# Kernel optimization log

Measured on AMD Instinct MI355X. Metric: run time of the kernel, lower is better.

The kernel has to match this reference:

```python
import jax, jax.numpy as jnp
import numpy as np

B, S, D_MODEL, D_OUT = 4, 4096, 512, 64


def setup_inputs() -> dict:
    key = jax.random.key(0)
    ks = jax.random.split(key, 10)
    query = jax.random.normal(ks[0], (B, S, D_MODEL), dtype=jnp.float32)
    key_t = jax.random.normal(ks[1], (B, S, D_MODEL), dtype=jnp.float32)
    value = jax.random.normal(ks[2], (B, S, D_MODEL), dtype=jnp.float32)
    mask = jax.random.randint(ks[3], (B, S, S), 0, 2, dtype=jnp.int32)
    sc = 1.0 / np.sqrt(D_MODEL)
    Wq = jax.random.uniform(ks[4], (D_MODEL, D_OUT), minval=-sc, maxval=sc, dtype=jnp.float32)
    bq = jnp.zeros((D_OUT,), dtype=jnp.float32)
    Wk = jax.random.uniform(ks[5], (D_MODEL, D_OUT), minval=-sc, maxval=sc, dtype=jnp.float32)
    bk = jnp.zeros((D_OUT,), dtype=jnp.float32)
    Wv = jax.random.uniform(ks[6], (D_MODEL, D_OUT), minval=-sc, maxval=sc, dtype=jnp.float32)
    bv = jnp.zeros((D_OUT,), dtype=jnp.float32)
    return {"query": query, "key": key_t, "value": value, "mask": mask,
            "Wq": Wq, "bq": bq, "Wk": Wk, "bk": bk, "Wv": Wv, "bv": bv}


def reference(query, key, value, mask, Wq, bq, Wk, bk, Wv, bv):
    # Linear projections (single head): [B,S,D_MODEL] @ [D_MODEL,D_OUT] + bias
    q = jnp.einsum('bsd,de->bse', query, Wq) + bq
    k = jnp.einsum('bsd,de->bse', key, Wk) + bk
    v = jnp.einsum('bsd,de->bse', value, Wv) + bv
    dim_k = k.shape[-1]
    scores = jnp.einsum('bqe,bke->bqk', q, k) / jnp.sqrt(jnp.float32(dim_k))  # [B,S,S]
    scores = jnp.where(mask == 0, -jnp.inf, scores)
    weights = jax.nn.softmax(scores, axis=-1)
    # dropout is identity in eval mode / for deterministic reference
    outputs = jnp.einsum('bqk,bke->bqe', weights, v)  # [B,S,D_OUT]
    return outputs
```

## Files before the change

kernel.cpp:

```cpp
#include <hip/hip_runtime.h>
#include <hip/hip_bf16.h>

#define BB 4
#define SS 4096
#define DMODEL 512
#define DOUT 64
#define NKH 2
#define KH (SS / NKH)
#define NIT (KH / 64)

typedef __bf16 bf16_t;
typedef __bf16 bf16x8 __attribute__((ext_vector_type(8)));
typedef float floatx4 __attribute__((ext_vector_type(4)));

__device__ inline void gl_lds16(const void* g, void* l) {
  __builtin_amdgcn_global_load_lds(
      (const __attribute__((address_space(1))) unsigned int*)g,
      (__attribute__((address_space(3))) unsigned int*)l, 16, 0, 0);
}

__global__ __launch_bounds__(256) void wtrans_kernel(
    const float* __restrict__ Wq, const float* __restrict__ Wk,
    const float* __restrict__ Wv, bf16_t* __restrict__ wT) {
  int idx = blockIdx.x * 256 + threadIdx.x;
  int mat = idx >> 12;
  int r   = idx & 4095;
  int e   = r & 63;
  int d0  = (r >> 6) << 3;
  const float* W = (mat == 0) ? Wq : ((mat == 1) ? Wk : Wv);
  bf16_t* dst = wT + (size_t)mat * (DOUT * DMODEL) + (size_t)e * DMODEL + d0;
#pragma unroll
  for (int j = 0; j < 8; ++j) dst[j] = (bf16_t)W[(size_t)(d0 + j) * DOUT + e];
}

__global__ __launch_bounds__(256) void proj_kernel(
    const float* __restrict__ inq, const float* __restrict__ ink,
    const float* __restrict__ inv, const bf16_t* __restrict__ wT,
    const float* __restrict__ bq, const float* __restrict__ bk,
    const float* __restrict__ bv,
    bf16_t* __restrict__ q_ws, bf16_t* __restrict__ k_ws,
    bf16_t* __restrict__ v_wsT) {
  const int mat = blockIdx.x >> 8;
  const int s0  = (blockIdx.x & 255) << 6;
  const int lane = threadIdx.x & 63;
  const int w    = threadIdx.x >> 6;
  const int col  = lane & 15, quad = lane >> 4;

  const float* inp  = (mat == 0) ? inq : ((mat == 1) ? ink : inv);
  const float* bias = (mat == 0) ? bq : ((mat == 1) ? bk : bv);
  const bf16_t* wt  = wT + (size_t)mat * (DOUT * DMODEL);

  const int arow = s0 + w * 16 + col;
  floatx4 acc[4] = {};

  for (int ch = 0; ch < 16; ++ch) {
    const int d0 = ch * 32 + quad * 8;
    float4 a0 = *(const float4*)(inp + (size_t)arow * DMODEL + d0);
    float4 a1 = *(const float4*)(inp + (size_t)arow * DMODEL + d0 + 4);
    bf16x8 af;
    af[0] = (bf16_t)a0.x; af[1] = (bf16_t)a0.y; af[2] = (bf16_t)a0.z; af[3] = (bf16_t)a0.w;
    af[4] = (bf16_t)a1.x; af[5] = (bf16_t)a1.y; af[6] = (bf16_t)a1.z; af[7] = (bf16_t)a1.w;
#pragma unroll
    for (int c = 0; c < 4; ++c) {
      bf16x8 bw = *(const bf16x8*)(wt + (size_t)(c * 16 + col) * DMODEL + d0);
      acc[c] = __builtin_amdgcn_mfma_f32_16x16x32_bf16(af, bw, acc[c], 0, 0, 0);
    }
  }

#pragma unroll
  for (int c = 0; c < 4; ++c) {
    float bcol = bias[c * 16 + col];
#pragma unroll
    for (int r = 0; r < 4; ++r) {
      int row = s0 + w * 16 + quad * 4 + r;
      float v = acc[c][r] + bcol;
      if (mat == 2) {
        int b = row >> 12, sp = row & 4095;
        v_wsT[((size_t)(b * DOUT + c * 16 + col)) * SS + sp] = (bf16_t)v;
      } else {
        bf16_t* dst = (mat == 0) ? q_ws : k_ws;
        dst[(size_t)row * DOUT + c * 16 + col] = (bf16_t)v;
      }
    }
  }
}

__global__ __launch_bounds__(256, 2) void attn_kernel(
    const bf16_t* __restrict__ q_ws, const bf16_t* __restrict__ k_ws,
    const bf16_t* __restrict__ v_wsT, const int* __restrict__ mask,
    float* __restrict__ O_part, float* __restrict__ l_part) {
  const int bq = blockIdx.x >> 1, kh = blockIdx.x & 1;
  const int b  = bq >> 6;
  const int q0 = (bq & 63) << 6;
  const int kbase = kh * KH;
  const int lane = threadIdx.x & 63;
  const int wi   = threadIdx.x >> 6;
  const int col  = lane & 15, quad = lane >> 4;

  __shared__ __align__(16) bf16_t Kb[2][64 * 64];
  __shared__ __align__(16) bf16_t Vb[2][64 * 64];
  __shared__ __align__(16) bf16_t Pl[4][16][72];

  const int qrowA = q0 + wi * 16 + col;
  const bf16_t* qbase = q_ws + ((size_t)(b * SS) + qrowA) * DOUT + quad * 8;
  const bf16x8 qa0 = *(const bf16x8*)(qbase);
  const bf16x8 qa1 = *(const bf16x8*)(qbase + 32);
  const int* mrow = mask + ((size_t)(b * SS) + qrowA) * SS + quad * 8;

  const int srow = lane >> 3;
  const int schk = (lane & 7) ^ srow;

  auto stage = [&](int it, int buf) {
    const int k0 = kbase + it * 64;
#pragma unroll
    for (int j = 0; j < 2; ++j) {
      const int i = wi * 2 + j;
      const int r = i * 8 + srow;
      const char* gK = (const char*)(k_ws + ((size_t)(b * SS) + k0 + r) * DOUT) + schk * 16;
      gl_lds16(gK, (char*)(&Kb[buf][0]) + i * 1024);
      const char* gV = (const char*)(v_wsT + ((size_t)(b * DOUT) + r) * SS + k0) + schk * 16;
      gl_lds16(gV, (char*)(&Vb[buf][0]) + i * 1024);
    }
  };

  int4 mc[2][2], mn[2][2];
  auto loadM = [&](int k0, int4 m[2][2]) {
#pragma unroll
    for (int s = 0; s < 2; ++s) {
      const int4* mp = (const int4*)(mrow + k0 + s * 32);
      m[s][0] = mp[0];
      m[s][1] = mp[1];
    }
  };

  floatx4 o[4] = {};
  float l_acc = 0.f;
  const bf16_t* prow_r = &Pl[wi][col][quad * 8];

  stage(0, 0);
  loadM(kbase, mc);
  __syncthreads();

  for (int it = 0; it < NIT; ++it) {
    const int buf = it & 1;
    const int itn = (it + 1 < NIT) ? it + 1 : it;

    loadM(kbase + itn * 64, mn);
    stage(itn, buf ^ 1);

    floatx4 sacc[4];
#pragma unroll
    for (int c = 0; c < 4; ++c) {
      const int row = c * 16 + col;
      bf16x8 k0f = *(const bf16x8*)((const char*)&Kb[buf][0] + row * 128 + ((quad ^ (col & 7)) * 16));
      bf16x8 k1f = *(const bf16x8*)((const char*)&Kb[buf][0] + row * 128 + (((4 | quad) ^ (col & 7)) * 16));
      floatx4 z = {};
      z = __builtin_amdgcn_mfma_f32_16x16x32_bf16(qa0, k0f, z, 0, 0, 0);
      z = __builtin_amdgcn_mfma_f32_16x16x32_bf16(qa1, k1f, z, 0, 0, 0);
      sacc[c] = z;
    }

    bf16x8 vc[4][2];
#pragma unroll
    for (int c = 0; c < 4; ++c) {
      const int row = c * 16 + col;
      vc[c][0] = *(const bf16x8*)((const char*)&Vb[buf][0] + row * 128 + ((quad ^ (col & 7)) * 16));
      vc[c][1] = *(const bf16x8*)((const char*)&Vb[buf][0] + row * 128 + (((4 | quad) ^ (col & 7)) * 16));
    }

#pragma unroll
    for (int c = 0; c < 4; ++c)
#pragma unroll
      for (int r = 0; r < 4; ++r)
        Pl[wi][quad * 4 + r][c * 16 + col] = (bf16_t)__expf(sacc[c][r] * 0.125f);

    asm volatile("s_waitcnt lgkmcnt(0)" ::: "memory");

    bf16x8 pa0 = *(const bf16x8*)(prow_r);
    bf16x8 pa1 = *(const bf16x8*)(prow_r + 32);

    float lp = 0.f;
    bf16x8 pm0, pm1;
    auto apply = [&](bf16x8 pa, int4 mlo, int4 mhi, bf16x8& pm) {
      int mm[8] = {mlo.x, mlo.y, mlo.z, mlo.w, mhi.x, mhi.y, mhi.z, mhi.w};
#pragma unroll
      for (int j = 0; j < 8; ++j) {
        bf16_t pv = (mm[j] != 0) ? pa[j] : (bf16_t)0.0f;
        pm[j] = pv;
        lp += (float)pv;
      }
    };
    apply(pa0, mc[0][0], mc[0][1], pm0);
    apply(pa1, mc[1][0], mc[1][1], pm1);
    lp += __shfl_xor(lp, 16);
    lp += __shfl_xor(lp, 32);
    l_acc += lp;

#pragma unroll
    for (int c = 0; c < 4; ++c) {
      o[c] = __builtin_amdgcn_mfma_f32_16x16x32_bf16(pm0, vc[c][0], o[c], 0, 0, 0);
      o[c] = __builtin_amdgcn_mfma_f32_16x16x32_bf16(pm1, vc[c][1], o[c], 0, 0, 0);
    }

    mc[0][0] = mn[0][0]; mc[0][1] = mn[0][1];
    mc[1][0] = mn[1][0]; mc[1][1] = mn[1][1];

    __syncthreads();
  }

  float* Op = O_part + (size_t)blockIdx.x * 64 * 64;
#pragma unroll
  for (int c = 0; c < 4; ++c)
#pragma unroll
    for (int r = 0; r < 4; ++r)
      Op[(wi * 16 + quad * 4 + r) * 64 + c * 16 + col] = o[c][r];
  if (quad == 0) l_part[(size_t)blockIdx.x * 64 + wi * 16 + col] = l_acc;
}

__global__ __launch_bounds__(256) void combine_kernel(
    const float* __restrict__ O_part, const float* __restrict__ l_part,
    float* __restrict__ out) {
  const int idx = blockIdx.x * 256 + threadIdx.x;
  const int base = idx * 4;
  const int row = base >> 6;
  const int c   = base & 63;
  const int t   = row >> 6;
  const int rl  = row & 63;
  const float* p0 = O_part + (((size_t)(t * 2 + 0) * 64 + rl) * 64 + c);
  const float* p1 = O_part + (((size_t)(t * 2 + 1) * 64 + rl) * 64 + c);
  const float inv = 1.0f / (l_part[(size_t)(t * 2) * 64 + rl] +
                            l_part[(size_t)(t * 2 + 1) * 64 + rl]);
  float4 a = *(const float4*)p0;
  float4 b = *(const float4*)p1;
  float4 r4 = {(a.x + b.x) * inv, (a.y + b.y) * inv,
               (a.z + b.z) * inv, (a.w + b.w) * inv};
  *(float4*)(out + base) = r4;
}

extern "C" void kernel_launch(void* const* d_in, const int* in_sizes, int n_in,
                              void* d_out, int out_size, void* d_ws, size_t ws_size,
                              hipStream_t stream) {
  const float* query = (const float*)d_in[0];
  const float* key   = (const float*)d_in[1];
  const float* value = (const float*)d_in[2];
  const int*   mask  = (const int*)d_in[3];
  const float* Wq = (const float*)d_in[4];
  const float* bq = (const float*)d_in[5];
  const float* Wk = (const float*)d_in[6];
  const float* bk = (const float*)d_in[7];
  const float* Wv = (const float*)d_in[8];
  const float* bv = (const float*)d_in[9];
  float* out = (float*)d_out;

  bf16_t* q_ws  = (bf16_t*)d_ws;
  bf16_t* k_ws  = q_ws + (size_t)BB * SS * DOUT;
  bf16_t* v_wsT = k_ws + (size_t)BB * SS * DOUT;
  bf16_t* wT    = v_wsT + (size_t)BB * SS * DOUT;
  float*  O_part = (float*)(wT + 3 * DOUT * DMODEL);
  float*  l_part = O_part + (size_t)512 * 64 * 64;

  hipLaunchKernelGGL(wtrans_kernel, dim3(48), dim3(256), 0, stream, Wq, Wk, Wv, wT);
  hipLaunchKernelGGL(proj_kernel, dim3(768), dim3(256), 0, stream,
                     query, key, value, wT, bq, bk, bv, q_ws, k_ws, v_wsT);
  hipLaunchKernelGGL(attn_kernel, dim3(512), dim3(256), 0, stream,
                     q_ws, k_ws, v_wsT, mask, O_part, l_part);
  hipLaunchKernelGGL(combine_kernel, dim3(1024), dim3(256), 0, stream,
                     O_part, l_part, out);
}
```

Measured before the change: 473.7 us.

## Keep P in registers via transposed QK MFMA, split keys four ways, prefetch proj inputs

The attention kernel now computes S^T with swapped MFMA operands, so each lane already holds the probabilities in the layout the PV MFMA needs. This removes the LDS round-trip for P, and V is stored with a permuted key order in the projection kernel to match. The key dimension is split into four parts instead of two, with occupancy hint 3, so more blocks run concurrently, and combine sums four partials. The projection kernel also software-prefetches the next input chunk; the extra partial outputs add workspace traffic.

```diff
diff --git a/kernel.cpp b/kernel.cpp
--- a/kernel.cpp
+++ b/kernel.cpp
@@ -5,7 +5,7 @@
 #define SS 4096
 #define DMODEL 512
 #define DOUT 64
-#define NKH 2
+#define NKH 4
 #define KH (SS / NKH)
 #define NIT (KH / 64)
 
@@ -51,12 +51,18 @@
   const bf16_t* wt  = wT + (size_t)mat * (DOUT * DMODEL);
 
   const int arow = s0 + w * 16 + col;
+  const float* arow_p = inp + (size_t)arow * DMODEL;
   floatx4 acc[4] = {};
 
+  float4 a0 = *(const float4*)(arow_p + quad * 8);
+  float4 a1 = *(const float4*)(arow_p + quad * 8 + 4);
+
   for (int ch = 0; ch < 16; ++ch) {
+    const int chn = (ch + 1 < 16) ? ch + 1 : ch;
+    float4 n0 = *(const float4*)(arow_p + chn * 32 + quad * 8);
+    float4 n1 = *(const float4*)(arow_p + chn * 32 + quad * 8 + 4);
+
     const int d0 = ch * 32 + quad * 8;
-    float4 a0 = *(const float4*)(inp + (size_t)arow * DMODEL + d0);
-    float4 a1 = *(const float4*)(inp + (size_t)arow * DMODEL + d0 + 4);
     bf16x8 af;
     af[0] = (bf16_t)a0.x; af[1] = (bf16_t)a0.y; af[2] = (bf16_t)a0.z; af[3] = (bf16_t)a0.w;
     af[4] = (bf16_t)a1.x; af[5] = (bf16_t)a1.y; af[6] = (bf16_t)a1.z; af[7] = (bf16_t)a1.w;
@@ -65,6 +71,7 @@
       bf16x8 bw = *(const bf16x8*)(wt + (size_t)(c * 16 + col) * DMODEL + d0);
       acc[c] = __builtin_amdgcn_mfma_f32_16x16x32_bf16(af, bw, acc[c], 0, 0, 0);
     }
+    a0 = n0; a1 = n1;
   }
 
 #pragma unroll
@@ -76,7 +83,10 @@
       float v = acc[c][r] + bcol;
       if (mat == 2) {
         int b = row >> 12, sp = row & 4095;
-        v_wsT[((size_t)(b * DOUT + c * 16 + col)) * SS + sp] = (bf16_t)v;
+        int kp = sp & 31;
+        int slot = ((kp & 12) << 1) | (kp & 3) | ((kp >> 4) << 2);
+        int sp2 = (sp & ~31) | slot;
+        v_wsT[((size_t)(b * DOUT + c * 16 + col)) * SS + sp2] = (bf16_t)v;
       } else {
         bf16_t* dst = (mat == 0) ? q_ws : k_ws;
         dst[(size_t)row * DOUT + c * 16 + col] = (bf16_t)v;
@@ -85,11 +95,11 @@
   }
 }
 
-__global__ __launch_bounds__(256, 2) void attn_kernel(
+__global__ __launch_bounds__(256, 3) void attn_kernel(
     const bf16_t* __restrict__ q_ws, const bf16_t* __restrict__ k_ws,
     const bf16_t* __restrict__ v_wsT, const int* __restrict__ mask,
     float* __restrict__ O_part, float* __restrict__ l_part) {
-  const int bq = blockIdx.x >> 1, kh = blockIdx.x & 1;
+  const int bq = blockIdx.x >> 2, kh = blockIdx.x & 3;
   const int b  = bq >> 6;
   const int q0 = (bq & 63) << 6;
   const int kbase = kh * KH;
@@ -99,13 +109,12 @@
 
   __shared__ __align__(16) bf16_t Kb[2][64 * 64];
   __shared__ __align__(16) bf16_t Vb[2][64 * 64];
-  __shared__ __align__(16) bf16_t Pl[4][16][72];
 
   const int qrowA = q0 + wi * 16 + col;
   const bf16_t* qbase = q_ws + ((size_t)(b * SS) + qrowA) * DOUT + quad * 8;
   const bf16x8 qa0 = *(const bf16x8*)(qbase);
   const bf16x8 qa1 = *(const bf16x8*)(qbase + 32);
-  const int* mrow = mask + ((size_t)(b * SS) + qrowA) * SS + quad * 8;
+  const int* mrow = mask + ((size_t)(b * SS) + qrowA) * SS + quad * 4;
 
   const int srow = lane >> 3;
   const int schk = (lane & 7) ^ srow;
@@ -123,19 +132,15 @@
     }
   };
 
-  int4 mc[2][2], mn[2][2];
-  auto loadM = [&](int k0, int4 m[2][2]) {
-#pragma unroll
-    for (int s = 0; s < 2; ++s) {
-      const int4* mp = (const int4*)(mrow + k0 + s * 32);
-      m[s][0] = mp[0];
-      m[s][1] = mp[1];
-    }
+  int4 mc[4], mn[4];
+  auto loadM = [&](int k0, int4 m[4]) {
+#pragma unroll
+    for (int c = 0; c < 4; ++c)
+      m[c] = *(const int4*)(mrow + k0 + c * 16);
   };
 
   floatx4 o[4] = {};
   float l_acc = 0.f;
-  const bf16_t* prow_r = &Pl[wi][col][quad * 8];
 
   stage(0, 0);
   loadM(kbase, mc);
@@ -155,8 +160,8 @@
       bf16x8 k0f = *(const bf16x8*)((const char*)&Kb[buf][0] + row * 128 + ((quad ^ (col & 7)) * 16));
       bf16x8 k1f = *(const bf16x8*)((const char*)&Kb[buf][0] + row * 128 + (((4 | quad) ^ (col & 7)) * 16));
       floatx4 z = {};
-      z = __builtin_amdgcn_mfma_f32_16x16x32_bf16(qa0, k0f, z, 0, 0, 0);
-      z = __builtin_amdgcn_mfma_f32_16x16x32_bf16(qa1, k1f, z, 0, 0, 0);
+      z = __builtin_amdgcn_mfma_f32_16x16x32_bf16(k0f, qa0, z, 0, 0, 0);
+      z = __builtin_amdgcn_mfma_f32_16x16x32_bf16(k1f, qa1, z, 0, 0, 0);
       sacc[c] = z;
     }
 
@@ -168,42 +173,33 @@
       vc[c][1] = *(const bf16x8*)((const char*)&Vb[buf][0] + row * 128 + (((4 | quad) ^ (col & 7)) * 16));
     }
 
-#pragma unroll
-    for (int c = 0; c < 4; ++c)
-#pragma unroll
-      for (int r = 0; r < 4; ++r)
-        Pl[wi][quad * 4 + r][c * 16 + col] = (bf16_t)__expf(sacc[c][r] * 0.125f);
-
-    asm volatile("s_waitcnt lgkmcnt(0)" ::: "memory");
-
-    bf16x8 pa0 = *(const bf16x8*)(prow_r);
-    bf16x8 pa1 = *(const bf16x8*)(prow_r + 32);
-
     float lp = 0.f;
-    bf16x8 pm0, pm1;
-    auto apply = [&](bf16x8 pa, int4 mlo, int4 mhi, bf16x8& pm) {
-      int mm[8] = {mlo.x, mlo.y, mlo.z, mlo.w, mhi.x, mhi.y, mhi.z, mhi.w};
-#pragma unroll
-      for (int j = 0; j < 8; ++j) {
-        bf16_t pv = (mm[j] != 0) ? pa[j] : (bf16_t)0.0f;
-        pm[j] = pv;
-        lp += (float)pv;
-      }
-    };
-    apply(pa0, mc[0][0], mc[0][1], pm0);
-    apply(pa1, mc[1][0], mc[1][1], pm1);
+    bf16x8 pa0, pa1;
+#pragma unroll
+    for (int c = 0; c < 4; ++c) {
+      const int4 m = mc[c];
+      float p0 = (m.x != 0) ? __expf(sacc[c][0] * 0.125f) : 0.f;
+      float p1 = (m.y != 0) ? __expf(sacc[c][1] * 0.125f) : 0.f;
+      float p2 = (m.z != 0) ? __expf(sacc[c][2] * 0.125f) : 0.f;
+      float p3 = (m.w != 0) ? __expf(sacc[c][3] * 0.125f) : 0.f;
+      lp += (p0 + p1) + (p2 + p3);
+      bf16x8& pa = (c < 2) ? pa0 : pa1;
+      const int off = (c & 1) * 4;
+      pa[off + 0] = (bf16_t)p0; pa[off + 1] = (bf16_t)p1;
+      pa[off + 2] = (bf16_t)p2; pa[off + 3] = (bf16_t)p3;
+    }
     lp += __shfl_xor(lp, 16);
     lp += __shfl_xor(lp, 32);
     l_acc += lp;
 
 #pragma unroll
     for (int c = 0; c < 4; ++c) {
-      o[c] = __builtin_amdgcn_mfma_f32_16x16x32_bf16(pm0, vc[c][0], o[c], 0, 0, 0);
-      o[c] = __builtin_amdgcn_mfma_f32_16x16x32_bf16(pm1, vc[c][1], o[c], 0, 0, 0);
-    }
-
-    mc[0][0] = mn[0][0]; mc[0][1] = mn[0][1];
-    mc[1][0] = mn[1][0]; mc[1][1] = mn[1][1];
+      o[c] = __builtin_amdgcn_mfma_f32_16x16x32_bf16(pa0, vc[c][0], o[c], 0, 0, 0);
+      o[c] = __builtin_amdgcn_mfma_f32_16x16x32_bf16(pa1, vc[c][1], o[c], 0, 0, 0);
+    }
+
+#pragma unroll
+    for (int c = 0; c < 4; ++c) mc[c] = mn[c];
 
     __syncthreads();
   }
@@ -226,14 +222,17 @@
   const int c   = base & 63;
   const int t   = row >> 6;
   const int rl  = row & 63;
-  const float* p0 = O_part + (((size_t)(t * 2 + 0) * 64 + rl) * 64 + c);
-  const float* p1 = O_part + (((size_t)(t * 2 + 1) * 64 + rl) * 64 + c);
-  const float inv = 1.0f / (l_part[(size_t)(t * 2) * 64 + rl] +
-                            l_part[(size_t)(t * 2 + 1) * 64 + rl]);
-  float4 a = *(const float4*)p0;
-  float4 b = *(const float4*)p1;
-  float4 r4 = {(a.x + b.x) * inv, (a.y + b.y) * inv,
-               (a.z + b.z) * inv, (a.w + b.w) * inv};
+  float4 s = {0.f, 0.f, 0.f, 0.f};
+  float lsum = 0.f;
+#pragma unroll
+  for (int p = 0; p < NKH; ++p) {
+    const float* pp = O_part + (((size_t)(t * NKH + p) * 64 + rl) * 64 + c);
+    float4 a = *(const float4*)pp;
+    s.x += a.x; s.y += a.y; s.z += a.z; s.w += a.w;
+    lsum += l_part[(size_t)(t * NKH + p) * 64 + rl];
+  }
+  const float inv = 1.0f / lsum;
+  float4 r4 = {s.x * inv, s.y * inv, s.z * inv, s.w * inv};
   *(float4*)(out + base) = r4;
 }
 
@@ -257,12 +256,12 @@
   bf16_t* v_wsT = k_ws + (size_t)BB * SS * DOUT;
   bf16_t* wT    = v_wsT + (size_t)BB * SS * DOUT;
   float*  O_part = (float*)(wT + 3 * DOUT * DMODEL);
-  float*  l_part = O_part + (size_t)512 * 64 * 64;
+  float*  l_part = O_part + (size_t)(BB * 64 * NKH) * 64 * 64;
 
   hipLaunchKernelGGL(wtrans_kernel, dim3(48), dim3(256), 0, stream, Wq, Wk, Wv, wT);
   hipLaunchKernelGGL(proj_kernel, dim3(768), dim3(256), 0, stream,
                      query, key, value, wT, bq, bk, bv, q_ws, k_ws, v_wsT);
-  hipLaunchKernelGGL(attn_kernel, dim3(512), dim3(256), 0, stream,
+  hipLaunchKernelGGL(attn_kernel, dim3(BB * 64 * NKH), dim3(256), 0, stream,
                      q_ws, k_ws, v_wsT, mask, O_part, l_part);
   hipLaunchKernelGGL(combine_kernel, dim3(1024), dim3(256), 0, stream,
                      O_part, l_part, out);
```

Measured after the change: 476.3 us. No clear change (+0.5%).
